# Kernel optimization log

Measured on AMD Instinct MI355X. Metric: run time of the kernel, lower is better.

The kernel has to match this reference:

```python
import jax, jax.numpy as jnp
import numpy as np

B, S, D, H = 4, 2048, 1024, 16
DK = D // H


def setup_inputs() -> dict:
    key = jax.random.key(0)
    k1, k2, k3, k4 = jax.random.split(key, 4)
    x = jax.random.normal(k1, (B, S, D), dtype=jnp.float32)
    # torch nn.Linear stores weight as [out, in]; y = x @ W.T + b
    w_qkv = jax.random.normal(k2, (3 * D, D), dtype=jnp.float32) * (1.0 / np.sqrt(D))
    b_qkv = jax.random.normal(k3, (3 * D,), dtype=jnp.float32) * 0.02
    w_o = jax.random.normal(k4, (D, D), dtype=jnp.float32) * (1.0 / np.sqrt(D))
    # causal mask: True where attention is disallowed (masked_fill semantics)
    mask = jnp.triu(jnp.ones((S, S), dtype=bool), k=1)[None, None]  # [1,1,S,S]
    return {"encodings_for_qkv": x, "mask": mask, "w_qkv": w_qkv, "b_qkv": b_qkv, "w_o": w_o}


def reference(encodings_for_qkv, mask, w_qkv, b_qkv, w_o):
    x = encodings_for_qkv
    qkv = x @ w_qkv.T + b_qkv                      # [B,S,3D]
    q, k, v = jnp.split(qkv, 3, axis=-1)           # each [B,S,D]

    def heads(t):
        return t.reshape(B, S, H, DK).transpose(0, 2, 1, 3)  # [B,H,S,DK]

    q, k, v = heads(q), heads(k), heads(v)
    scale = 1.0 / np.sqrt(DK).astype(np.float32)
    sims = jnp.einsum('bhqd,bhkd->bhqk', q, k) * scale       # [B,H,S,S]
    sims = jnp.where(mask, jnp.float32(-1e9), sims)
    attn = jax.nn.softmax(sims, axis=-1)
    out = jnp.einsum('bhqk,bhkd->bhqd', attn, v)             # [B,H,S,DK]
    out = out.transpose(0, 2, 1, 3).reshape(B, S, D)
    return out @ w_o.T
```

## Files before the change

### kernel.cpp

```cpp
#include <hip/hip_runtime.h>
#include <hip/hip_bf16.h>

typedef __attribute__((ext_vector_type(8))) __bf16 bf16x8;
typedef __attribute__((ext_vector_type(4))) __bf16 bf16x4;
typedef __attribute__((ext_vector_type(4))) float f32x4;

constexpr int B = 4, S = 2048, D = 1024, H = 16, DK = 64;

#define GLOAD16(gp, lp)                                                              \
  __builtin_amdgcn_global_load_lds((const __attribute__((address_space(1))) void*)(gp), \
                                   (__attribute__((address_space(3))) void*)(lp), 16, 0, 0)

__global__ __launch_bounds__(256) void convert_bf16(const float* __restrict__ X,
                                                    const float* __restrict__ Wqkv,
                                                    const float* __restrict__ Wo,
                                                    __bf16* __restrict__ Xb,
                                                    __bf16* __restrict__ Wqkvb,
                                                    __bf16* __restrict__ Wob) {
  const int NX = B * S * D;
  const int NW = 3 * D * D;
  const int NO = D * D;
  const int total8 = (NX + NW + NO) / 8;
  for (int i = blockIdx.x * blockDim.x + threadIdx.x; i < total8;
       i += gridDim.x * blockDim.x) {
    const int e = i * 8;
    const float* src;
    __bf16* dst;
    int off;
    if (e < NX) {
      src = X; dst = Xb; off = e;
    } else if (e < NX + NW) {
      src = Wqkv; dst = Wqkvb; off = e - NX;
    } else {
      src = Wo; dst = Wob; off = e - NX - NW;
    }
    float4 a = *reinterpret_cast<const float4*>(src + off);
    float4 b = *reinterpret_cast<const float4*>(src + off + 4);
    bf16x8 v = {(__bf16)a.x, (__bf16)a.y, (__bf16)a.z, (__bf16)a.w,
                (__bf16)b.x, (__bf16)b.y, (__bf16)b.z, (__bf16)b.w};
    *reinterpret_cast<bf16x8*>(dst + off) = v;
  }
}

__global__ __launch_bounds__(256) void qkv_gemm(const __bf16* __restrict__ Xb,
                                                const __bf16* __restrict__ Wb,
                                                const float* __restrict__ bias,
                                                __bf16* __restrict__ Qb,
                                                __bf16* __restrict__ Kb,
                                                __bf16* __restrict__ VTb) {
  __shared__ __bf16 As[128 * 64];
  __shared__ __bf16 Bs[128 * 64];
  const int tid = threadIdx.x;
  const int lane = tid & 63;
  const int w = tid >> 6;
  const int wr = w >> 1, wc = w & 1;
  const int lr = lane & 15, lb = lane >> 4;
  const int m0 = blockIdx.x * 128, n0 = blockIdx.y * 128;

  int srow[4], sgcol[4];
#pragma unroll
  for (int rnd = 0; rnd < 4; ++rnd) {
    const int i = rnd * 256 + tid;
    srow[rnd] = i >> 3;
    sgcol[rnd] = ((i & 7) ^ (srow[rnd] & 7)) << 3;
  }

  f32x4 acc[4][4];
#pragma unroll
  for (int i = 0; i < 4; ++i)
#pragma unroll
    for (int j = 0; j < 4; ++j) acc[i][j] = f32x4{0.f, 0.f, 0.f, 0.f};

  for (int k0 = 0; k0 < D; k0 += 64) {
#pragma unroll
    for (int rnd = 0; rnd < 4; ++rnd) {
      GLOAD16(&Xb[(size_t)(m0 + srow[rnd]) * D + k0 + sgcol[rnd]],
              (char*)As + rnd * 4096 + w * 1024);
      GLOAD16(&Wb[(size_t)(n0 + srow[rnd]) * D + k0 + sgcol[rnd]],
              (char*)Bs + rnd * 4096 + w * 1024);
    }
    __syncthreads();

    bf16x8 af[4][2], bfr[4][2];
#pragma unroll
    for (int m = 0; m < 4; ++m) {
      const int row = wr * 64 + m * 16 + lr;
#pragma unroll
      for (int ks = 0; ks < 2; ++ks)
        af[m][ks] = *reinterpret_cast<const bf16x8*>(
            (const char*)As + row * 128 + (((ks * 32 + lb * 8) << 1) ^ ((row & 7) << 4)));
    }
#pragma unroll
    for (int n = 0; n < 4; ++n) {
      const int row = wc * 64 + n * 16 + lr;
#pragma unroll
      for (int ks = 0; ks < 2; ++ks)
        bfr[n][ks] = *reinterpret_cast<const bf16x8*>(
            (const char*)Bs + row * 128 + (((ks * 32 + lb * 8) << 1) ^ ((row & 7) << 4)));
    }
#pragma unroll
    for (int m = 0; m < 4; ++m)
#pragma unroll
      for (int n = 0; n < 4; ++n) {
        acc[m][n] = __builtin_amdgcn_mfma_f32_16x16x32_bf16(af[m][0], bfr[n][0], acc[m][n], 0, 0, 0);
        acc[m][n] = __builtin_amdgcn_mfma_f32_16x16x32_bf16(af[m][1], bfr[n][1], acc[m][n], 0, 0, 0);
      }
    __syncthreads();
  }

  const int seg = n0 >> 10;
#pragma unroll
  for (int m = 0; m < 4; ++m)
#pragma unroll
    for (int n = 0; n < 4; ++n) {
      const int c = n0 + wc * 64 + n * 16 + lr;
      const int cc = c & 1023;
      const int h = cc >> 6, dk = cc & 63;
      const float bv = bias[c];
#pragma unroll
      for (int r = 0; r < 4; ++r) {
        const int t = m0 + wr * 64 + m * 16 + lb * 4 + r;
        const int bb = t >> 11;
        const int s = t & 2047;
        const float v = acc[m][n][r] + bv;
        const size_t bh = (size_t)bb * H + h;
        if (seg == 0)
          Qb[(bh * S + s) * DK + dk] = (__bf16)(v * 0.180336893f);
        else if (seg == 1)
          Kb[(bh * S + s) * DK + dk] = (__bf16)v;
        else
          VTb[(bh * DK + dk) * S + s] = (__bf16)v;
      }
    }
}

__global__ __launch_bounds__(256) void attn_fwd(const __bf16* __restrict__ Qb,
                                                const __bf16* __restrict__ Kb,
                                                const __bf16* __restrict__ VTb,
                                                __bf16* __restrict__ AO) {
  __shared__ __bf16 Kl[64 * 64];
  __shared__ __bf16 Vl[64 * 64];
  __shared__ __bf16 Ps[4][32][72];
  const int tid = threadIdx.x;
  const int lane = tid & 63;
  const int w = tid >> 6;
  const int lr = lane & 15, lb = lane >> 4;

  const int flat = blockIdx.x;
  const int xcd = flat & 7;
  const int idx = flat >> 3;
  const int hg = idx & 7;
  const int pr = idx >> 3;
  const int bh = hg * 8 + xcd;
  const int bb = bh >> 4, h = bh & 15;

  const __bf16* Q = Qb + (size_t)bh * S * DK;
  const __bf16* K = Kb + (size_t)bh * S * DK;
  const __bf16* VT = VTb + (size_t)bh * DK * S;

  const int srow = tid >> 2;
  const int scol = (tid & 3) * 16;
  const int sbyte = srow * 128 + scol * 2;
  const int sswz = (srow & 7) << 4;
  const int rsw = (lr & 7) << 4;

  bf16x8 ones;
#pragma unroll
  for (int i = 0; i < 8; ++i) ones[i] = (__bf16)1.0f;

  for (int pass = 0; pass < 2; ++pass) {
    const int qt = pass ? (15 - pr) : pr;
    const int q0 = qt * 128 + w * 32;
    const int nt = 2 * qt + 2;
    const int ntw = 2 * qt + 1 + (w >> 1);

    bf16x8 qf[2][2];
#pragma unroll
    for (int m = 0; m < 2; ++m)
#pragma unroll
      for (int d = 0; d < 2; ++d)
        qf[m][d] = *reinterpret_cast<const bf16x8*>(
            &Q[(size_t)(q0 + m * 16 + lr) * DK + d * 32 + lb * 8]);

    {
      const __bf16* Kg = K + (size_t)srow * DK + scol;
      bf16x8 k0 = *reinterpret_cast<const bf16x8*>(Kg);
      bf16x8 k1 = *reinterpret_cast<const bf16x8*>(Kg + 8);
      const __bf16* Vg = VT + (size_t)srow * S + scol;
      bf16x8 v0 = *reinterpret_cast<const bf16x8*>(Vg);
      bf16x8 v1 = *reinterpret_cast<const bf16x8*>(Vg + 8);
      char* kd = (char*)&Kl[0];
      char* vd = (char*)&Vl[0];
      *reinterpret_cast<bf16x8*>(kd + (sbyte ^ sswz)) = k0;
      *reinterpret_cast<bf16x8*>(kd + ((sbyte + 16) ^ sswz)) = k1;
      *reinterpret_cast<bf16x8*>(vd + (sbyte ^ sswz)) = v0;
      *reinterpret_cast<bf16x8*>(vd + ((sbyte + 16) ^ sswz)) = v1;
    }
    __syncthreads();

    f32x4 o[2][4], lsum[2];
#pragma unroll
    for (int m = 0; m < 2; ++m) {
#pragma unroll
      for (int n = 0; n < 4; ++n) o[m][n] = f32x4{0.f, 0.f, 0.f, 0.f};
      lsum[m] = f32x4{0.f, 0.f, 0.f, 0.f};
    }
    float mrun[2];
#pragma unroll
    for (int m = 0; m < 2; ++m) mrun[m] = -1e30f;

    for (int t = 0; t < nt; ++t) {
      const int kv0 = t * 64;
      const bool have_next = (t + 1 < nt);
      bf16x8 gk0, gk1, gv0, gv1;
      if (have_next) {
        const __bf16* Kg = K + ((size_t)(kv0 + 64) + srow) * DK + scol;
        gk0 = *reinterpret_cast<const bf16x8*>(Kg);
        gk1 = *reinterpret_cast<const bf16x8*>(Kg + 8);
        const __bf16* Vg = VT + (size_t)srow * S + (kv0 + 64) + scol;
        gv0 = *reinterpret_cast<const bf16x8*>(Vg);
        gv1 = *reinterpret_cast<const bf16x8*>(Vg + 8);
      }

      if (t < ntw) {
        const char* kbase = (const char*)&Kl[0];
        const char* vbase = (const char*)&Vl[0];
        bf16x8 kf[4][2];
#pragma unroll
        for (int kc = 0; kc < 4; ++kc)
#pragma unroll
          for (int d = 0; d < 2; ++d)
            kf[kc][d] = *reinterpret_cast<const bf16x8*>(
                kbase + (kc * 16 + lr) * 128 + ((d * 64 + lb * 16) ^ rsw));

        f32x4 st[2][4];
        __builtin_amdgcn_s_setprio(1);
#pragma unroll
        for (int m = 0; m < 2; ++m)
#pragma unroll
          for (int kc = 0; kc < 4; ++kc) {
            f32x4 z = f32x4{0.f, 0.f, 0.f, 0.f};
            z = __builtin_amdgcn_mfma_f32_16x16x32_bf16(kf[kc][0], qf[m][0], z, 0, 0, 0);
            z = __builtin_amdgcn_mfma_f32_16x16x32_bf16(kf[kc][1], qf[m][1], z, 0, 0, 0);
            st[m][kc] = z;
          }
        __builtin_amdgcn_s_setprio(0);

        if (t == ntw - 1) {
#pragma unroll
          for (int m = 0; m < 2; ++m) {
            const int qg = q0 + m * 16 + lr;
#pragma unroll
            for (int kc = 0; kc < 4; ++kc)
#pragma unroll
              for (int r = 0; r < 4; ++r) {
                const int kg = kv0 + kc * 16 + 4 * lb + r;
                if (kg > qg) st[m][kc][r] = -1e30f;
              }
          }
        }

#pragma unroll
        for (int m = 0; m < 2; ++m) {
          float a0 = fmaxf(fmaxf(st[m][0][0], st[m][0][1]), fmaxf(st[m][0][2], st[m][0][3]));
          float a1 = fmaxf(fmaxf(st[m][1][0], st[m][1][1]), fmaxf(st[m][1][2], st[m][1][3]));
          float a2 = fmaxf(fmaxf(st[m][2][0], st[m][2][1]), fmaxf(st[m][2][2], st[m][2][3]));
          float a3 = fmaxf(fmaxf(st[m][3][0], st[m][3][1]), fmaxf(st[m][3][2], st[m][3][3]));
          float mx = fmaxf(fmaxf(a0, a1), fmaxf(a2, a3));
          mx = fmaxf(mx, __shfl_xor(mx, 16, 64));
          mx = fmaxf(mx, __shfl_xor(mx, 32, 64));

          if (__any(mx > mrun[m] + 11.f)) {
            const float nm = fmaxf(mrun[m], mx);
            const float alpha = exp2f(mrun[m] - nm);
            mrun[m] = nm;
#pragma unroll
            for (int r = 0; r < 4; ++r) {
              const float ao = __shfl(alpha, 4 * lb + r, 64);
#pragma unroll
              for (int n = 0; n < 4; ++n) o[m][n][r] *= ao;
              lsum[m][r] *= ao;
            }
          }

#pragma unroll
          for (int kc = 0; kc < 4; ++kc) {
            bf16x4 pk;
#pragma unroll
            for (int r = 0; r < 4; ++r) pk[r] = (__bf16)exp2f(st[m][kc][r] - mrun[m]);
            *reinterpret_cast<bf16x4*>(&Ps[w][m * 16 + lr][kc * 16 + 4 * lb]) = pk;
          }
        }

        asm volatile("s_waitcnt lgkmcnt(0)" ::: "memory");
        __builtin_amdgcn_sched_barrier(0);

        bf16x8 pa[2][2];
#pragma unroll
        for (int m = 0; m < 2; ++m)
#pragma unroll
          for (int ks = 0; ks < 2; ++ks)
            pa[m][ks] = *reinterpret_cast<const bf16x8*>(&Ps[w][m * 16 + lr][ks * 32 + lb * 8]);
        bf16x8 vf[4][2];
#pragma unroll
        for (int n = 0; n < 4; ++n)
#pragma unroll
          for (int ks = 0; ks < 2; ++ks)
            vf[n][ks] = *reinterpret_cast<const bf16x8*>(
                vbase + (n * 16 + lr) * 128 + ((ks * 64 + lb * 16) ^ rsw));

        __builtin_amdgcn_s_setprio(1);
#pragma unroll
        for (int m = 0; m < 2; ++m) {
#pragma unroll
          for (int n = 0; n < 4; ++n) {
            o[m][n] = __builtin_amdgcn_mfma_f32_16x16x32_bf16(pa[m][0], vf[n][0], o[m][n], 0, 0, 0);
            o[m][n] = __builtin_amdgcn_mfma_f32_16x16x32_bf16(pa[m][1], vf[n][1], o[m][n], 0, 0, 0);
          }
          lsum[m] = __builtin_amdgcn_mfma_f32_16x16x32_bf16(pa[m][0], ones, lsum[m], 0, 0, 0);
          lsum[m] = __builtin_amdgcn_mfma_f32_16x16x32_bf16(pa[m][1], ones, lsum[m], 0, 0, 0);
        }
        __builtin_amdgcn_s_setprio(0);
      }

      __syncthreads();
      if (have_next) {
        char* kd = (char*)&Kl[0];
        char* vd = (char*)&Vl[0];
        *reinterpret_cast<bf16x8*>(kd + (sbyte ^ sswz)) = gk0;
        *reinterpret_cast<bf16x8*>(kd + ((sbyte + 16) ^ sswz)) = gk1;
        *reinterpret_cast<bf16x8*>(vd + (sbyte ^ sswz)) = gv0;
        *reinterpret_cast<bf16x8*>(vd + ((sbyte + 16) ^ sswz)) = gv1;
      }
      __syncthreads();
    }

#pragma unroll
    for (int m = 0; m < 2; ++m)
#pragma unroll
      for (int r = 0; r < 4; ++r) {
        const float inv = 1.f / lsum[m][r];
        const int q = q0 + m * 16 + 4 * lb + r;
#pragma unroll
        for (int n = 0; n < 4; ++n)
          AO[((size_t)(bb * S + q)) * D + h * DK + n * 16 + lr] = (__bf16)(o[m][n][r] * inv);
      }
  }
}

__global__ __launch_bounds__(256) void out_gemm(const __bf16* __restrict__ AOp,
                                                const __bf16* __restrict__ Wb,
                                                float* __restrict__ Out) {
  __shared__ __bf16 As[128 * 64];
  __shared__ __bf16 Bs[128 * 64];
  const int tid = threadIdx.x;
  const int lane = tid & 63;
  const int w = tid >> 6;
  const int wr = w >> 1, wc = w & 1;
  const int lr = lane & 15, lb = lane >> 4;
  const int m0 = blockIdx.x * 128, n0 = blockIdx.y * 128;

  int srow[4], sgcol[4];
#pragma unroll
  for (int rnd = 0; rnd < 4; ++rnd) {
    const int i = rnd * 256 + tid;
    srow[rnd] = i >> 3;
    sgcol[rnd] = ((i & 7) ^ (srow[rnd] & 7)) << 3;
  }

  f32x4 acc[4][4];
#pragma unroll
  for (int i = 0; i < 4; ++i)
#pragma unroll
    for (int j = 0; j < 4; ++j) acc[i][j] = f32x4{0.f, 0.f, 0.f, 0.f};

  for (int k0 = 0; k0 < D; k0 += 64) {
#pragma unroll
    for (int rnd = 0; rnd < 4; ++rnd) {
      GLOAD16(&AOp[(size_t)(m0 + srow[rnd]) * D + k0 + sgcol[rnd]],
              (char*)As + rnd * 4096 + w * 1024);
      GLOAD16(&Wb[(size_t)(n0 + srow[rnd]) * D + k0 + sgcol[rnd]],
              (char*)Bs + rnd * 4096 + w * 1024);
    }
    __syncthreads();

    bf16x8 af[4][2], bfr[4][2];
#pragma unroll
    for (int m = 0; m < 4; ++m) {
      const int row = wr * 64 + m * 16 + lr;
#pragma unroll
      for (int ks = 0; ks < 2; ++ks)
        af[m][ks] = *reinterpret_cast<const bf16x8*>(
            (const char*)As + row * 128 + (((ks * 32 + lb * 8) << 1) ^ ((row & 7) << 4)));
    }
#pragma unroll
    for (int n = 0; n < 4; ++n) {
      const int row = wc * 64 + n * 16 + lr;
#pragma unroll
      for (int ks = 0; ks < 2; ++ks)
        bfr[n][ks] = *reinterpret_cast<const bf16x8*>(
            (const char*)Bs + row * 128 + (((ks * 32 + lb * 8) << 1) ^ ((row & 7) << 4)));
    }
#pragma unroll
    for (int m = 0; m < 4; ++m)
#pragma unroll
      for (int n = 0; n < 4; ++n) {
        acc[m][n] = __builtin_amdgcn_mfma_f32_16x16x32_bf16(af[m][0], bfr[n][0], acc[m][n], 0, 0, 0);
        acc[m][n] = __builtin_amdgcn_mfma_f32_16x16x32_bf16(af[m][1], bfr[n][1], acc[m][n], 0, 0, 0);
      }
    __syncthreads();
  }

#pragma unroll
  for (int m = 0; m < 4; ++m)
#pragma unroll
    for (int n = 0; n < 4; ++n)
#pragma unroll
      for (int r = 0; r < 4; ++r)
        Out[(size_t)(m0 + wr * 64 + m * 16 + lb * 4 + r) * D + n0 + wc * 64 + n * 16 + lr] =
            acc[m][n][r];
}

extern "C" void kernel_launch(void* const* d_in, const int* in_sizes, int n_in,
                              void* d_out, int out_size, void* d_ws, size_t ws_size,
                              hipStream_t stream) {
  (void)in_sizes; (void)n_in; (void)out_size; (void)ws_size;
  const float* x = (const float*)d_in[0];
  const float* w_qkv = (const float*)d_in[2];
  const float* b_qkv = (const float*)d_in[3];
  const float* w_o = (const float*)d_in[4];
  float* out = (float*)d_out;

  const size_t qkv_elems = (size_t)B * H * S * DK;
  __bf16* Qb = (__bf16*)d_ws;
  __bf16* Kb = Qb + qkv_elems;
  __bf16* VTb = Kb + qkv_elems;
  __bf16* AO = VTb + qkv_elems;
  __bf16* Xb = AO + qkv_elems;
  __bf16* Wqkvb = Xb + (size_t)B * S * D;
  __bf16* Wob = Wqkvb + (size_t)3 * D * D;

  convert_bf16<<<2048, 256, 0, stream>>>(x, w_qkv, w_o, Xb, Wqkvb, Wob);
  qkv_gemm<<<dim3(64, 24), 256, 0, stream>>>(Xb, Wqkvb, b_qkv, Qb, Kb, VTb);
  attn_fwd<<<dim3(8 * (B * H)), 256, 0, stream>>>(Qb, Kb, VTb, AO);
  out_gemm<<<dim3(64, 8), 256, 0, stream>>>(AO, Wob, out);
}
```

Baseline: 204.3 us.

## Load K/V fragments directly from global memory, dropping shared staging and block barriers

The attention kernel no longer stages K and V tiles through shared memory with per-tile __syncthreads. Each wave now loads its K and V^T MFMA fragments straight from global memory (relying on cache reuse across the four waves) and runs only its own causal tile count, with no idle waiting on other waves. Launch bounds now request two blocks per CU. This removes barrier stalls and the LDS round trip, but it multiplies global/L2 traffic by the wave count and loses the register prefetch of the next tile, so load latency is more exposed.

After: 243.3 us. +19.1%, slower.

```diff
diff --git a/kernel.cpp b/kernel.cpp
--- a/kernel.cpp
+++ b/kernel.cpp
@@ -134,12 +134,10 @@
     }
 }
 
-__global__ __launch_bounds__(256) void attn_fwd(const __bf16* __restrict__ Qb,
-                                                const __bf16* __restrict__ Kb,
-                                                const __bf16* __restrict__ VTb,
-                                                __bf16* __restrict__ AO) {
-  __shared__ __bf16 Kl[64 * 64];
-  __shared__ __bf16 Vl[64 * 64];
+__global__ __launch_bounds__(256, 2) void attn_fwd(const __bf16* __restrict__ Qb,
+                                                   const __bf16* __restrict__ Kb,
+                                                   const __bf16* __restrict__ VTb,
+                                                   __bf16* __restrict__ AO) {
   __shared__ __bf16 Ps[4][32][72];
   const int tid = threadIdx.x;
   const int lane = tid & 63;
@@ -158,12 +156,6 @@
   const __bf16* K = Kb + (size_t)bh * S * DK;
   const __bf16* VT = VTb + (size_t)bh * DK * S;
 
-  const int srow = tid >> 2;
-  const int scol = (tid & 3) * 16;
-  const int sbyte = srow * 128 + scol * 2;
-  const int sswz = (srow & 7) << 4;
-  const int rsw = (lr & 7) << 4;
-
   bf16x8 ones;
 #pragma unroll
   for (int i = 0; i < 8; ++i) ones[i] = (__bf16)1.0f;
@@ -171,7 +163,6 @@
   for (int pass = 0; pass < 2; ++pass) {
     const int qt = pass ? (15 - pr) : pr;
     const int q0 = qt * 128 + w * 32;
-    const int nt = 2 * qt + 2;
     const int ntw = 2 * qt + 1 + (w >> 1);
 
     bf16x8 qf[2][2];
@@ -182,22 +173,6 @@
         qf[m][d] = *reinterpret_cast<const bf16x8*>(
             &Q[(size_t)(q0 + m * 16 + lr) * DK + d * 32 + lb * 8]);
 
-    {
-      const __bf16* Kg = K + (size_t)srow * DK + scol;
-      bf16x8 k0 = *reinterpret_cast<const bf16x8*>(Kg);
-      bf16x8 k1 = *reinterpret_cast<const bf16x8*>(Kg + 8);
-      const __bf16* Vg = VT + (size_t)srow * S + scol;
-      bf16x8 v0 = *reinterpret_cast<const bf16x8*>(Vg);
-      bf16x8 v1 = *reinterpret_cast<const bf16x8*>(Vg + 8);
-      char* kd = (char*)&Kl[0];
-      char* vd = (char*)&Vl[0];
-      *reinterpret_cast<bf16x8*>(kd + (sbyte ^ sswz)) = k0;
-      *reinterpret_cast<bf16x8*>(kd + ((sbyte + 16) ^ sswz)) = k1;
-      *reinterpret_cast<bf16x8*>(vd + (sbyte ^ sswz)) = v0;
-      *reinterpret_cast<bf16x8*>(vd + ((sbyte + 16) ^ sswz)) = v1;
-    }
-    __syncthreads();
-
     f32x4 o[2][4], lsum[2];
 #pragma unroll
     for (int m = 0; m < 2; ++m) {
@@ -209,130 +184,103 @@
 #pragma unroll
     for (int m = 0; m < 2; ++m) mrun[m] = -1e30f;
 
-    for (int t = 0; t < nt; ++t) {
+    for (int t = 0; t < ntw; ++t) {
       const int kv0 = t * 64;
-      const bool have_next = (t + 1 < nt);
-      bf16x8 gk0, gk1, gv0, gv1;
-      if (have_next) {
-        const __bf16* Kg = K + ((size_t)(kv0 + 64) + srow) * DK + scol;
-        gk0 = *reinterpret_cast<const bf16x8*>(Kg);
-        gk1 = *reinterpret_cast<const bf16x8*>(Kg + 8);
-        const __bf16* Vg = VT + (size_t)srow * S + (kv0 + 64) + scol;
-        gv0 = *reinterpret_cast<const bf16x8*>(Vg);
-        gv1 = *reinterpret_cast<const bf16x8*>(Vg + 8);
-      }
-
-      if (t < ntw) {
-        const char* kbase = (const char*)&Kl[0];
-        const char* vbase = (const char*)&Vl[0];
-        bf16x8 kf[4][2];
-#pragma unroll
-        for (int kc = 0; kc < 4; ++kc)
-#pragma unroll
-          for (int d = 0; d < 2; ++d)
-            kf[kc][d] = *reinterpret_cast<const bf16x8*>(
-                kbase + (kc * 16 + lr) * 128 + ((d * 64 + lb * 16) ^ rsw));
-
-        f32x4 st[2][4];
-        __builtin_amdgcn_s_setprio(1);
-#pragma unroll
-        for (int m = 0; m < 2; ++m)
-#pragma unroll
-          for (int kc = 0; kc < 4; ++kc) {
-            f32x4 z = f32x4{0.f, 0.f, 0.f, 0.f};
-            z = __builtin_amdgcn_mfma_f32_16x16x32_bf16(kf[kc][0], qf[m][0], z, 0, 0, 0);
-            z = __builtin_amdgcn_mfma_f32_16x16x32_bf16(kf[kc][1], qf[m][1], z, 0, 0, 0);
-            st[m][kc] = z;
+      bf16x8 kf[4][2], vf[4][2];
+#pragma unroll
+      for (int kc = 0; kc < 4; ++kc)
+#pragma unroll
+        for (int d = 0; d < 2; ++d)
+          kf[kc][d] = *reinterpret_cast<const bf16x8*>(
+              &K[(size_t)(kv0 + kc * 16 + lr) * DK + d * 32 + lb * 8]);
+#pragma unroll
+      for (int n = 0; n < 4; ++n)
+#pragma unroll
+        for (int ks = 0; ks < 2; ++ks)
+          vf[n][ks] = *reinterpret_cast<const bf16x8*>(
+              &VT[(size_t)(n * 16 + lr) * S + kv0 + ks * 32 + lb * 8]);
+
+      f32x4 st[2][4];
+      __builtin_amdgcn_s_setprio(1);
+#pragma unroll
+      for (int m = 0; m < 2; ++m)
+#pragma unroll
+        for (int kc = 0; kc < 4; ++kc) {
+          f32x4 z = f32x4{0.f, 0.f, 0.f, 0.f};
+          z = __builtin_amdgcn_mfma_f32_16x16x32_bf16(kf[kc][0], qf[m][0], z, 0, 0, 0);
+          z = __builtin_amdgcn_mfma_f32_16x16x32_bf16(kf[kc][1], qf[m][1], z, 0, 0, 0);
+          st[m][kc] = z;
+        }
+      __builtin_amdgcn_s_setprio(0);
+
+      if (t == ntw - 1) {
+#pragma unroll
+        for (int m = 0; m < 2; ++m) {
+          const int qg = q0 + m * 16 + lr;
+#pragma unroll
+          for (int kc = 0; kc < 4; ++kc)
+#pragma unroll
+            for (int r = 0; r < 4; ++r) {
+              const int kg = kv0 + kc * 16 + 4 * lb + r;
+              if (kg > qg) st[m][kc][r] = -1e30f;
+            }
+        }
+      }
+
+#pragma unroll
+      for (int m = 0; m < 2; ++m) {
+        float a0 = fmaxf(fmaxf(st[m][0][0], st[m][0][1]), fmaxf(st[m][0][2], st[m][0][3]));
+        float a1 = fmaxf(fmaxf(st[m][1][0], st[m][1][1]), fmaxf(st[m][1][2], st[m][1][3]));
+        float a2 = fmaxf(fmaxf(st[m][2][0], st[m][2][1]), fmaxf(st[m][2][2], st[m][2][3]));
+        float a3 = fmaxf(fmaxf(st[m][3][0], st[m][3][1]), fmaxf(st[m][3][2], st[m][3][3]));
+        float mx = fmaxf(fmaxf(a0, a1), fmaxf(a2, a3));
+        mx = fmaxf(mx, __shfl_xor(mx, 16, 64));
+        mx = fmaxf(mx, __shfl_xor(mx, 32, 64));
+
+        if (__any(mx > mrun[m] + 11.f)) {
+          const float nm = fmaxf(mrun[m], mx);
+          const float alpha = exp2f(mrun[m] - nm);
+          mrun[m] = nm;
+#pragma unroll
+          for (int r = 0; r < 4; ++r) {
+            const float ao = __shfl(alpha, 4 * lb + r, 64);
+#pragma unroll
+            for (int n = 0; n < 4; ++n) o[m][n][r] *= ao;
+            lsum[m][r] *= ao;
           }
-        __builtin_amdgcn_s_setprio(0);
-
-        if (t == ntw - 1) {
-#pragma unroll
-          for (int m = 0; m < 2; ++m) {
-            const int qg = q0 + m * 16 + lr;
-#pragma unroll
-            for (int kc = 0; kc < 4; ++kc)
-#pragma unroll
-              for (int r = 0; r < 4; ++r) {
-                const int kg = kv0 + kc * 16 + 4 * lb + r;
-                if (kg > qg) st[m][kc][r] = -1e30f;
-              }
-          }
-        }
-
-#pragma unroll
-        for (int m = 0; m < 2; ++m) {
-          float a0 = fmaxf(fmaxf(st[m][0][0], st[m][0][1]), fmaxf(st[m][0][2], st[m][0][3]));
-          float a1 = fmaxf(fmaxf(st[m][1][0], st[m][1][1]), fmaxf(st[m][1][2], st[m][1][3]));
-          float a2 = fmaxf(fmaxf(st[m][2][0], st[m][2][1]), fmaxf(st[m][2][2], st[m][2][3]));
-          float a3 = fmaxf(fmaxf(st[m][3][0], st[m][3][1]), fmaxf(st[m][3][2], st[m][3][3]));
-          float mx = fmaxf(fmaxf(a0, a1), fmaxf(a2, a3));
-          mx = fmaxf(mx, __shfl_xor(mx, 16, 64));
-          mx = fmaxf(mx, __shfl_xor(mx, 32, 64));
-
-          if (__any(mx > mrun[m] + 11.f)) {
-            const float nm = fmaxf(mrun[m], mx);
-            const float alpha = exp2f(mrun[m] - nm);
-            mrun[m] = nm;
-#pragma unroll
-            for (int r = 0; r < 4; ++r) {
-              const float ao = __shfl(alpha, 4 * lb + r, 64);
-#pragma unroll
-              for (int n = 0; n < 4; ++n) o[m][n][r] *= ao;
-              lsum[m][r] *= ao;
-            }
-          }
-
-#pragma unroll
-          for (int kc = 0; kc < 4; ++kc) {
-            bf16x4 pk;
-#pragma unroll
-            for (int r = 0; r < 4; ++r) pk[r] = (__bf16)exp2f(st[m][kc][r] - mrun[m]);
-            *reinterpret_cast<bf16x4*>(&Ps[w][m * 16 + lr][kc * 16 + 4 * lb]) = pk;
-          }
-        }
-
-        asm volatile("s_waitcnt lgkmcnt(0)" ::: "memory");
-        __builtin_amdgcn_sched_barrier(0);
-
-        bf16x8 pa[2][2];
-#pragma unroll
-        for (int m = 0; m < 2; ++m)
-#pragma unroll
-          for (int ks = 0; ks < 2; ++ks)
-            pa[m][ks] = *reinterpret_cast<const bf16x8*>(&Ps[w][m * 16 + lr][ks * 32 + lb * 8]);
-        bf16x8 vf[4][2];
-#pragma unroll
-        for (int n = 0; n < 4; ++n)
-#pragma unroll
-          for (int ks = 0; ks < 2; ++ks)
-            vf[n][ks] = *reinterpret_cast<const bf16x8*>(
-                vbase + (n * 16 + lr) * 128 + ((ks * 64 + lb * 16) ^ rsw));
-
-        __builtin_amdgcn_s_setprio(1);
-#pragma unroll
-        for (int m = 0; m < 2; ++m) {
-#pragma unroll
-          for (int n = 0; n < 4; ++n) {
-            o[m][n] = __builtin_amdgcn_mfma_f32_16x16x32_bf16(pa[m][0], vf[n][0], o[m][n], 0, 0, 0);
-            o[m][n] = __builtin_amdgcn_mfma_f32_16x16x32_bf16(pa[m][1], vf[n][1], o[m][n], 0, 0, 0);
-          }
-          lsum[m] = __builtin_amdgcn_mfma_f32_16x16x32_bf16(pa[m][0], ones, lsum[m], 0, 0, 0);
-          lsum[m] = __builtin_amdgcn_mfma_f32_16x16x32_bf16(pa[m][1], ones, lsum[m], 0, 0, 0);
-        }
-        __builtin_amdgcn_s_setprio(0);
-      }
-
-      __syncthreads();
-      if (have_next) {
-        char* kd = (char*)&Kl[0];
-        char* vd = (char*)&Vl[0];
-        *reinterpret_cast<bf16x8*>(kd + (sbyte ^ sswz)) = gk0;
-        *reinterpret_cast<bf16x8*>(kd + ((sbyte + 16) ^ sswz)) = gk1;
-        *reinterpret_cast<bf16x8*>(vd + (sbyte ^ sswz)) = gv0;
-        *reinterpret_cast<bf16x8*>(vd + ((sbyte + 16) ^ sswz)) = gv1;
-      }
-      __syncthreads();
+        }
+
+#pragma unroll
+        for (int kc = 0; kc < 4; ++kc) {
+          bf16x4 pk;
+#pragma unroll
+          for (int r = 0; r < 4; ++r) pk[r] = (__bf16)exp2f(st[m][kc][r] - mrun[m]);
+          *reinterpret_cast<bf16x4*>(&Ps[w][m * 16 + lr][kc * 16 + 4 * lb]) = pk;
+        }
+      }
+
+      asm volatile("s_waitcnt lgkmcnt(0)" ::: "memory");
+      __builtin_amdgcn_sched_barrier(0);
+
+      bf16x8 pa[2][2];
+#pragma unroll
+      for (int m = 0; m < 2; ++m)
+#pragma unroll
+        for (int ks = 0; ks < 2; ++ks)
+          pa[m][ks] = *reinterpret_cast<const bf16x8*>(&Ps[w][m * 16 + lr][ks * 32 + lb * 8]);
+
+      __builtin_amdgcn_s_setprio(1);
+#pragma unroll
+      for (int m = 0; m < 2; ++m) {
+#pragma unroll
+        for (int n = 0; n < 4; ++n) {
+          o[m][n] = __builtin_amdgcn_mfma_f32_16x16x32_bf16(pa[m][0], vf[n][0], o[m][n], 0, 0, 0);
+          o[m][n] = __builtin_amdgcn_mfma_f32_16x16x32_bf16(pa[m][1], vf[n][1], o[m][n], 0, 0, 0);
+        }
+        lsum[m] = __builtin_amdgcn_mfma_f32_16x16x32_bf16(pa[m][0], ones, lsum[m], 0, 0, 0);
+        lsum[m] = __builtin_amdgcn_mfma_f32_16x16x32_bf16(pa[m][1], ones, lsum[m], 0, 0, 0);
+      }
+      __builtin_amdgcn_s_setprio(0);
     }
 
 #pragma unroll
```
